# Kernel tuning notes

Hardware: AMD Instinct MI355X
Metric: run time of the kernel (lower is better)

Reference implementation:

```python
import jax, jax.numpy as jnp
import numpy as np

EMBED_DIM = 512
NUM_HEADS = 8
HEAD_DIM = EMBED_DIM // NUM_HEADS


def setup_inputs() -> dict:
    key = jax.random.key(0)
    k1, k2, kw, kb, kow, kob = jax.random.split(key, 6)
    B, L, C = 2, 2048, EMBED_DIM
    s = 1.0 / np.sqrt(C)
    return {
        "x1": jax.random.normal(k1, (B, L, C), dtype=jnp.float32),
        "x2": jax.random.normal(k2, (B, L, C), dtype=jnp.float32),
        # nn.Linear(embed_dim, 3*embed_dim): weight [3C, C], bias [3C]
        "qkv_w": jax.random.uniform(kw, (3 * C, C), jnp.float32, -s, s),
        "qkv_b": jax.random.uniform(kb, (3 * C,), jnp.float32, -s, s),
        # nn.Linear(embed_dim, embed_dim): weight [C, C], bias [C]
        "out_w": jax.random.uniform(kow, (C, C), jnp.float32, -s, s),
        "out_b": jax.random.uniform(kob, (C,), jnp.float32, -s, s),
    }


def _qkv(x, qkv_w, qkv_b):
    B, L, C = x.shape
    H, D = NUM_HEADS, C // NUM_HEADS
    # Linear: x @ W^T + b, then view(B, L, H, 3, D) and split along the '3' axis
    qkv = (jnp.einsum("blc,fc->blf", x, qkv_w) + qkv_b).reshape(B, L, H, 3, D)
    qkv = jnp.transpose(qkv, (3, 0, 2, 1, 4))  # [3, B, H, L, D]
    return qkv[0], qkv[1], qkv[2]


def _attend(q, k, v):
    # q,k,v: [B, H, L, D]; scale by 1/sqrt(D)
    scale = 1.0 / np.sqrt(q.shape[-1]).astype(np.float32)
    scores = jnp.einsum("bhqd,bhkd->bhqk", q, k) * scale  # [B,H,L,L]
    attn = jax.nn.softmax(scores, axis=-1)
    out = jnp.einsum("bhqk,bhkd->bhqd", attn, v)
    B, H, L, D = out.shape
    return jnp.transpose(out, (0, 2, 1, 3)).reshape(B, L, H * D)


def reference(x1, x2, qkv_w, qkv_b, out_w, out_b):
    q1, k1, v1 = _qkv(x1, qkv_w, qkv_b)
    q2, k2, v2 = _qkv(x2, qkv_w, qkv_b)
    out1 = _attend(q1, k2, v2)  # q from x1, k/v from x2
    out2 = _attend(q2, k1, v1)  # q from x2, k/v from x1
    out1 = jnp.einsum("blc,fc->blf", out1, out_w) + out_b
    out2 = jnp.einsum("blc,fc->blf", out2, out_w) + out_b
    return (out1, out2)
```

## Files before the change

kernel.cpp:

```cpp
#include <hip/hip_runtime.h>
#include <stdint.h>

typedef unsigned short u16;
typedef unsigned int u32;
typedef short bf16x8 __attribute__((ext_vector_type(8)));
typedef float f32x4 __attribute__((ext_vector_type(4)));
typedef float f32x16 __attribute__((ext_vector_type(16)));

#define K_DIM 512

__device__ __forceinline__ u16 f2bf(float f) {
  union { float f; u32 u; } v; v.f = f;
  return (u16)((v.u + 0x8000u) >> 16);
}
__device__ __forceinline__ u32 pk2(float lo, float hi) {
  union { float f; u32 u; } a, b; a.f = lo; b.f = hi;
  return __builtin_amdgcn_perm(b.u + 0x8000u, a.u + 0x8000u, 0x07060302u);
}

__global__ void cvt_kernel(const float* __restrict__ x1, const float* __restrict__ x2,
                           const float* __restrict__ qkvw, const float* __restrict__ outw,
                           u16* __restrict__ xb, u16* __restrict__ wqkv, u16* __restrict__ wout) {
  int tid = blockIdx.x * 256 + threadIdx.x;
  const float4* src; u16* dst; int idx = tid;
  if (idx < 524288)        { src = (const float4*)x1;   dst = xb; }
  else if (idx < 1048576)  { src = (const float4*)x2;   dst = xb + 2097152; idx -= 524288; }
  else if (idx < 1245184)  { src = (const float4*)qkvw; dst = wqkv;         idx -= 1048576; }
  else                     { src = (const float4*)outw; dst = wout;         idx -= 1245184; }
  float4 v = src[idx];
  *(uint2*)&dst[idx * 4] = make_uint2(pk2(v.x, v.y), pk2(v.z, v.w));
}

#define LDA 40

__global__ __launch_bounds__(256, 3) void qkv_gemm(
    const u16* __restrict__ A, const u16* __restrict__ W, const float* __restrict__ bias,
    u16* __restrict__ qb, u16* __restrict__ kb, u16* __restrict__ vtb) {
  __shared__ __align__(16) u16 As[2][128 * LDA];
  __shared__ __align__(16) u16 Bs[2][128 * LDA];
  const int t = threadIdx.x;
  const int m0 = blockIdx.x * 128, n0 = blockIdx.y * 128;
  const int lane = t & 63, l16 = lane & 15, quad = lane >> 4;
  const int w = t >> 6;
  const int wm = (w >> 1) * 64, wn = (w & 1) * 64;
  const int sr = t >> 2, sc = (t & 3) * 8;

  const u16* Ap = A + (size_t)(m0 + sr) * K_DIM + sc;
  const u16* Wp = W + (size_t)(n0 + sr) * K_DIM + sc;

  f32x4 acc[4][4];
#pragma unroll
  for (int i = 0; i < 4; ++i)
#pragma unroll
    for (int j = 0; j < 4; ++j) acc[i][j] = (f32x4){0.f, 0.f, 0.f, 0.f};

  uint4 ra0 = *(const uint4*)(Ap);
  uint4 ra1 = *(const uint4*)(Ap + 64 * K_DIM);
  uint4 rb0 = *(const uint4*)(Wp);
  uint4 rb1 = *(const uint4*)(Wp + 64 * K_DIM);
  *(uint4*)&As[0][sr * LDA + sc] = ra0;
  *(uint4*)&As[0][(sr + 64) * LDA + sc] = ra1;
  *(uint4*)&Bs[0][sr * LDA + sc] = rb0;
  *(uint4*)&Bs[0][(sr + 64) * LDA + sc] = rb1;
  ra0 = *(const uint4*)(Ap + 32);
  ra1 = *(const uint4*)(Ap + 64 * K_DIM + 32);
  rb0 = *(const uint4*)(Wp + 32);
  rb1 = *(const uint4*)(Wp + 64 * K_DIM + 32);
  __syncthreads();

  for (int kt = 0; kt < 16; ++kt) {
    const int cur = kt & 1, nxt = cur ^ 1;
    if (kt < 15) {
      *(uint4*)&As[nxt][sr * LDA + sc] = ra0;
      *(uint4*)&As[nxt][(sr + 64) * LDA + sc] = ra1;
      *(uint4*)&Bs[nxt][sr * LDA + sc] = rb0;
      *(uint4*)&Bs[nxt][(sr + 64) * LDA + sc] = rb1;
    }
    if (kt < 14) {
      int ko = (kt + 2) * 32;
      ra0 = *(const uint4*)(Ap + ko);
      ra1 = *(const uint4*)(Ap + 64 * K_DIM + ko);
      rb0 = *(const uint4*)(Wp + ko);
      rb1 = *(const uint4*)(Wp + 64 * K_DIM + ko);
    }
    bf16x8 af[4], bfr[4];
#pragma unroll
    for (int mi = 0; mi < 4; ++mi)
      af[mi] = *(const bf16x8*)&As[cur][(wm + mi * 16 + l16) * LDA + quad * 8];
#pragma unroll
    for (int ni = 0; ni < 4; ++ni)
      bfr[ni] = *(const bf16x8*)&Bs[cur][(wn + ni * 16 + l16) * LDA + quad * 8];
#pragma unroll
    for (int mi = 0; mi < 4; ++mi)
#pragma unroll
      for (int ni = 0; ni < 4; ++ni)
        acc[mi][ni] = __builtin_amdgcn_mfma_f32_16x16x32_bf16(bfr[ni], af[mi], acc[mi][ni], 0, 0, 0);
    __syncthreads();
  }

  const int fbase = n0 + wn;
  const int h = fbase / 192;
  const int s = (fbase - h * 192) >> 6;
  float4 bv[4];
#pragma unroll
  for (int ni = 0; ni < 4; ++ni)
    bv[ni] = *(const float4*)&bias[fbase + ni * 16 + quad * 4];
  const int bh = m0 >> 11;
  const int lbase = (m0 & 2047) + wm;

  if (s == 2) {
    u16* dst = vtb + (size_t)((bh * 8 + h) * 64) * 2048;
#pragma unroll
    for (int mi = 0; mi < 4; ++mi) {
      int l = lbase + mi * 16 + l16;
#pragma unroll
      for (int ni = 0; ni < 4; ++ni)
#pragma unroll
        for (int r = 0; r < 4; ++r)
          dst[(ni * 16 + quad * 4 + r) * 2048 + l] = f2bf(acc[mi][ni][r] + bv[ni][r]);
    }
  } else {
    u16* dst = (s == 0 ? qb : kb) + (size_t)((bh * 8 + h) * 2048) * 64;
    const float sc2 = (s == 0) ? 0.18033688011112042f : 1.0f;
#pragma unroll
    for (int mi = 0; mi < 4; ++mi) {
      int l = lbase + mi * 16 + l16;
#pragma unroll
      for (int ni = 0; ni < 4; ++ni) {
        float v0 = (acc[mi][ni][0] + bv[ni][0]) * sc2;
        float v1 = (acc[mi][ni][1] + bv[ni][1]) * sc2;
        float v2 = (acc[mi][ni][2] + bv[ni][2]) * sc2;
        float v3 = (acc[mi][ni][3] + bv[ni][3]) * sc2;
        *(uint2*)&dst[(size_t)l * 64 + ni * 16 + quad * 4] = make_uint2(pk2(v0, v1), pk2(v2, v3));
      }
    }
  }
}

#define LQ 72

#define SPHASE(SS, KBUF)                                                          \
  do {                                                                            \
    _Pragma("unroll") for (int r_ = 0; r_ < 16; ++r_) SS[r_] = 0.f;               \
    _Pragma("unroll") for (int ks_ = 0; ks_ < 4; ++ks_) {                         \
      bf16x8 kfr = *(const bf16x8*)&Ks[KBUF][(half32 + l32) * LQ + ks_ * 16 + h2 * 8]; \
      SS = __builtin_amdgcn_mfma_f32_32x32x16_bf16(kfr, qf[ks_], SS, 0, 0, 0);    \
    }                                                                             \
  } while (0)

#define SOFTPV(SS, VBUF)                                                          \
  do {                                                                            \
    float p[16];                                                                  \
    _Pragma("unroll") for (int r_ = 0; r_ < 16; ++r_)                             \
      p[r_] = __builtin_amdgcn_exp2f(SS[r_]);                                     \
    _Pragma("unroll") for (int r_ = 0; r_ < 16; r_ += 4)                          \
      rs += (p[r_] + p[r_ + 1]) + (p[r_ + 2] + p[r_ + 3]);                        \
    u32 a0 = pk2(p[0], p[1]),   b0 = pk2(p[2], p[3]);                             \
    u32 c0 = pk2(p[4], p[5]),   d0 = pk2(p[6], p[7]);                             \
    u32 a1 = pk2(p[8], p[9]),   b1 = pk2(p[10], p[11]);                           \
    u32 c1 = pk2(p[12], p[13]), d1 = pk2(p[14], p[15]);                           \
    asm("v_permlane32_swap_b32 %0, %1" : "+v"(a0), "+v"(c0));                     \
    asm("v_permlane32_swap_b32 %0, %1" : "+v"(b0), "+v"(d0));                     \
    asm("v_permlane32_swap_b32 %0, %1" : "+v"(a1), "+v"(c1));                     \
    asm("v_permlane32_swap_b32 %0, %1" : "+v"(b1), "+v"(d1));                     \
    union { u32 u[4]; bf16x8 v; } f0_, f1_;                                       \
    f0_.u[0] = a0; f0_.u[1] = b0; f0_.u[2] = c0; f0_.u[3] = d0;                   \
    f1_.u[0] = a1; f1_.u[1] = b1; f1_.u[2] = c1; f1_.u[3] = d1;                   \
    bf16x8 pf0 = f0_.v, pf1 = f1_.v;                                              \
    const u16* vb_ = (const u16*)VTs + (VBUF) * (64 * LQ);                        \
    bf16x8 vf0 = *(const bf16x8*)&vb_[l32 * LQ + half32 + h2 * 8];                \
    bf16x8 vf1 = *(const bf16x8*)&vb_[(32 + l32) * LQ + half32 + h2 * 8];         \
    oacc[0] = __builtin_amdgcn_mfma_f32_32x32x16_bf16(vf0, pf0, oacc[0], 0, 0, 0);\
    oacc[1] = __builtin_amdgcn_mfma_f32_32x32x16_bf16(vf1, pf0, oacc[1], 0, 0, 0);\
    vf0 = *(const bf16x8*)&vb_[l32 * LQ + half32 + 16 + h2 * 8];                  \
    vf1 = *(const bf16x8*)&vb_[(32 + l32) * LQ + half32 + 16 + h2 * 8];           \
    oacc[0] = __builtin_amdgcn_mfma_f32_32x32x16_bf16(vf0, pf1, oacc[0], 0, 0, 0);\
    oacc[1] = __builtin_amdgcn_mfma_f32_32x32x16_bf16(vf1, pf1, oacc[1], 0, 0, 0);\
  } while (0)

__global__ __launch_bounds__(512, 4) void attn_kernel(
    const u16* __restrict__ qb, const u16* __restrict__ kb, const u16* __restrict__ vtb,
    u16* __restrict__ attnb) {
  __shared__ __align__(16) u16 Ks[2][64 * LQ];
  __shared__ __align__(16) u16 VTs[4][64 * LQ];

  const int t = threadIdx.x;
  const int w = t >> 6, lane = t & 63, l32 = lane & 31, h2 = lane >> 5;
  const int qg = w & 3, half32 = (w >> 2) * 32;
  const int bid = blockIdx.x;
  const int comb = bid & 31;
  const int qt = bid >> 5;
  const int h = comb & 7, bb = (comb >> 3) & 1, pair = comb >> 4;
  const int in_q = pair, in_kv = pair ^ 1;

  const u16* Qg = qb + (size_t)((in_q * 2 + bb) * 8 + h) * 2048 * 64;
  const u16* Kg = kb + (size_t)((in_kv * 2 + bb) * 8 + h) * 2048 * 64;
  const u16* Vg = vtb + (size_t)((in_kv * 2 + bb) * 8 + h) * 64 * 2048;

  const int srow = t >> 3, sseg = (t & 7) * 8;
  uint4 rk0 = *(const uint4*)(Kg + srow * 64 + sseg);
  uint4 rv0 = *(const uint4*)(Vg + srow * 2048 + sseg);

  bf16x8 qf[4];
#pragma unroll
  for (int ks = 0; ks < 4; ++ks)
    qf[ks] = *(const bf16x8*)(Qg + (qt * 128 + qg * 32 + l32) * 64 + ks * 16 + h2 * 8);

  auto stage = [&](int kbuf, int vbuf) {
    *(uint4*)&Ks[kbuf][srow * LQ + sseg] = rk0;
    *(uint4*)&VTs[vbuf][srow * LQ + sseg] = rv0;
  };
  auto gload = [&](int kt) {
    const int ko = kt * 64;
    rk0 = *(const uint4*)(Kg + (ko + srow) * 64 + sseg);
    rv0 = *(const uint4*)(Vg + srow * 2048 + ko + sseg);
  };

  f32x16 oacc[2];
#pragma unroll
  for (int mi = 0; mi < 2; ++mi)
#pragma unroll
    for (int r = 0; r < 16; ++r) oacc[mi][r] = 0.f;
  float rs = 0.f;
  f32x16 sA, sB;

  stage(0, 0);
  gload(1);
  __syncthreads();

  SPHASE(sA, 0);
  stage(1, 1);
  gload(2);
  __syncthreads();

#pragma unroll 1
  for (int it = 0; it < 16; ++it) {
    const int e = (it & 1) << 1;
    SPHASE(sB, 1);
    SOFTPV(sA, e);
    if (it == 15) break;
    stage(0, e ^ 2);
    gload(2 * it + 3);
    __syncthreads();
    SPHASE(sA, 0);
    SOFTPV(sB, e + 1);
    stage(1, e ^ 3);
    if (it < 14) gload(2 * it + 4);
    __syncthreads();
  }
  SOFTPV(sB, 3);

  rs += __shfl_xor(rs, 32);
  __syncthreads();
  float* red = (float*)&VTs[0][0];
  float* rsb = red + 4 * 64 * 32;
  if (half32) {
#pragma unroll
    for (int mi = 0; mi < 2; ++mi)
#pragma unroll
      for (int r = 0; r < 16; ++r) {
        int d = mi * 32 + (r & 3) + 8 * (r >> 2) + 4 * h2;
        red[(qg * 64 + d) * 32 + l32] = oacc[mi][r];
      }
    if (lane < 32) rsb[qg * 32 + l32] = rs;
  }
  __syncthreads();
  if (!half32) {
#pragma unroll
    for (int mi = 0; mi < 2; ++mi)
#pragma unroll
      for (int r = 0; r < 16; ++r) {
        int d = mi * 32 + (r & 3) + 8 * (r >> 2) + 4 * h2;
        oacc[mi][r] += red[(qg * 64 + d) * 32 + l32];
      }
    rs += rsb[qg * 32 + l32];
    const float inv = 1.0f / rs;
    const int row = in_q * 4096 + bb * 2048 + qt * 128 + qg * 32 + l32;
#pragma unroll
    for (int mi = 0; mi < 2; ++mi)
#pragma unroll
      for (int rg = 0; rg < 4; ++rg) {
        float v0 = oacc[mi][rg * 4 + 0] * inv;
        float v1 = oacc[mi][rg * 4 + 1] * inv;
        float v2 = oacc[mi][rg * 4 + 2] * inv;
        float v3 = oacc[mi][rg * 4 + 3] * inv;
        *(uint2*)&attnb[(size_t)row * 512 + h * 64 + mi * 32 + rg * 8 + h2 * 4] =
            make_uint2(pk2(v0, v1), pk2(v2, v3));
      }
  }
}

__global__ __launch_bounds__(256, 2) void out_gemm(
    const u16* __restrict__ A, const u16* __restrict__ W, const float* __restrict__ bias,
    float* __restrict__ out) {
  __shared__ __align__(16) u16 As[2][64 * LDA];
  __shared__ __align__(16) u16 Bs[2][128 * LDA];
  const int t = threadIdx.x;
  const int m0 = blockIdx.x * 64, n0 = blockIdx.y * 128;
  const int lane = t & 63, l16 = lane & 15, quad = lane >> 4;
  const int w = t >> 6;
  const int wm = (w & 1) * 32, wn = (w >> 1) * 64;
  const int ar = t >> 2, ac = (t & 3) * 8;
  const int sr = t >> 2, sc = (t & 3) * 8;

  const u16* Ap = A + (size_t)(m0 + ar) * K_DIM + ac;
  const u16* Wp = W + (size_t)(n0 + sr) * K_DIM + sc;

  f32x4 acc[2][4];
#pragma unroll
  for (int i = 0; i < 2; ++i)
#pragma unroll
    for (int j = 0; j < 4; ++j) acc[i][j] = (f32x4){0.f, 0.f, 0.f, 0.f};

  uint4 ra = *(const uint4*)Ap;
  uint4 rb0 = *(const uint4*)(Wp);
  uint4 rb1 = *(const uint4*)(Wp + 64 * K_DIM);
  *(uint4*)&As[0][ar * LDA + ac] = ra;
  *(uint4*)&Bs[0][sr * LDA + sc] = rb0;
  *(uint4*)&Bs[0][(sr + 64) * LDA + sc] = rb1;
  ra = *(const uint4*)(Ap + 32);
  rb0 = *(const uint4*)(Wp + 32);
  rb1 = *(const uint4*)(Wp + 64 * K_DIM + 32);
  __syncthreads();

  for (int kt = 0; kt < 16; ++kt) {
    const int cur = kt & 1, nxt = cur ^ 1;
    if (kt < 15) {
      *(uint4*)&As[nxt][ar * LDA + ac] = ra;
      *(uint4*)&Bs[nxt][sr * LDA + sc] = rb0;
      *(uint4*)&Bs[nxt][(sr + 64) * LDA + sc] = rb1;
    }
    if (kt < 14) {
      int ko = (kt + 2) * 32;
      ra = *(const uint4*)(Ap + ko);
      rb0 = *(const uint4*)(Wp + ko);
      rb1 = *(const uint4*)(Wp + 64 * K_DIM + ko);
    }
    bf16x8 af[2], bfr[4];
#pragma unroll
    for (int mi = 0; mi < 2; ++mi)
      af[mi] = *(const bf16x8*)&As[cur][(wm + mi * 16 + l16) * LDA + quad * 8];
#pragma unroll
    for (int ni = 0; ni < 4; ++ni)
      bfr[ni] = *(const bf16x8*)&Bs[cur][(wn + ni * 16 + l16) * LDA + quad * 8];
#pragma unroll
    for (int mi = 0; mi < 2; ++mi)
#pragma unroll
      for (int ni = 0; ni < 4; ++ni)
        acc[mi][ni] = __builtin_amdgcn_mfma_f32_16x16x32_bf16(af[mi], bfr[ni], acc[mi][ni], 0, 0, 0);
    __syncthreads();
  }

#pragma unroll
  for (int ni = 0; ni < 4; ++ni) {
    int f = n0 + wn + ni * 16 + l16;
    float bv = bias[f];
#pragma unroll
    for (int mi = 0; mi < 2; ++mi)
#pragma unroll
      for (int r = 0; r < 4; ++r) {
        int m = m0 + wm + mi * 16 + quad * 4 + r;
        out[(size_t)m * 512 + f] = acc[mi][ni][r] + bv;
      }
  }
}

extern "C" void kernel_launch(void* const* d_in, const int* in_sizes, int n_in,
                              void* d_out, int out_size, void* d_ws, size_t ws_size,
                              hipStream_t stream) {
  const float* x1   = (const float*)d_in[0];
  const float* x2   = (const float*)d_in[1];
  const float* qkvw = (const float*)d_in[2];
  const float* qkvb = (const float*)d_in[3];
  const float* outw = (const float*)d_in[4];
  const float* outb = (const float*)d_in[5];
  float* out = (float*)d_out;
  char* ws = (char*)d_ws;

  u16* xb    = (u16*)(ws + 0);
  u16* wqkv  = (u16*)(ws + 8388608);
  u16* wout  = (u16*)(ws + 9961472);
  u16* qb    = (u16*)(ws + 10485760);
  u16* kb    = (u16*)(ws + 18874368);
  u16* vtb   = (u16*)(ws + 27262976);
  u16* attnb = (u16*)(ws + 0);

  cvt_kernel<<<5120, 256, 0, stream>>>(x1, x2, qkvw, outw, xb, wqkv, wout);

  dim3 g1(64, 12);
  qkv_gemm<<<g1, 256, 0, stream>>>(xb, wqkv, qkvb, qb, kb, vtb);

  attn_kernel<<<512, 512, 0, stream>>>(qb, kb, vtb, attnb);

  dim3 g3(128, 4);
  out_gemm<<<g3, 256, 0, stream>>>(attnb, wout, outb, out);
}
```

Measured before the change: 158.6 us.

## Load K fragments directly from global into registers, drop K shared staging

```diff
diff --git a/kernel.cpp b/kernel.cpp
--- a/kernel.cpp
+++ b/kernel.cpp
@@ -139,13 +139,20 @@
 
 #define LQ 72
 
-#define SPHASE(SS, KBUF)                                                          \
+#define LOADK(KF, KT)                                                             \
+  do {                                                                            \
+    const u16* kp_ = Kg + ((KT) * 64 + half32 + l32) * 64 + h2 * 8;               \
+    KF[0] = *(const bf16x8*)(kp_);                                                \
+    KF[1] = *(const bf16x8*)(kp_ + 16);                                           \
+    KF[2] = *(const bf16x8*)(kp_ + 32);                                           \
+    KF[3] = *(const bf16x8*)(kp_ + 48);                                           \
+  } while (0)
+
+#define SPHASE(SS, KF)                                                            \
   do {                                                                            \
     _Pragma("unroll") for (int r_ = 0; r_ < 16; ++r_) SS[r_] = 0.f;               \
-    _Pragma("unroll") for (int ks_ = 0; ks_ < 4; ++ks_) {                         \
-      bf16x8 kfr = *(const bf16x8*)&Ks[KBUF][(half32 + l32) * LQ + ks_ * 16 + h2 * 8]; \
-      SS = __builtin_amdgcn_mfma_f32_32x32x16_bf16(kfr, qf[ks_], SS, 0, 0, 0);    \
-    }                                                                             \
+    _Pragma("unroll") for (int ks_ = 0; ks_ < 4; ++ks_)                           \
+      SS = __builtin_amdgcn_mfma_f32_32x32x16_bf16(KF[ks_], qf[ks_], SS, 0, 0, 0);\
   } while (0)
 
 #define SOFTPV(SS, VBUF)                                                          \
@@ -181,7 +188,6 @@
 __global__ __launch_bounds__(512, 4) void attn_kernel(
     const u16* __restrict__ qb, const u16* __restrict__ kb, const u16* __restrict__ vtb,
     u16* __restrict__ attnb) {
-  __shared__ __align__(16) u16 Ks[2][64 * LQ];
   __shared__ __align__(16) u16 VTs[4][64 * LQ];
 
   const int t = threadIdx.x;
@@ -198,22 +204,22 @@
   const u16* Vg = vtb + (size_t)((in_kv * 2 + bb) * 8 + h) * 64 * 2048;
 
   const int srow = t >> 3, sseg = (t & 7) * 8;
-  uint4 rk0 = *(const uint4*)(Kg + srow * 64 + sseg);
   uint4 rv0 = *(const uint4*)(Vg + srow * 2048 + sseg);
+
+  bf16x8 kfA[4], kfB[4];
+  LOADK(kfA, 0);
+  LOADK(kfB, 1);
 
   bf16x8 qf[4];
 #pragma unroll
   for (int ks = 0; ks < 4; ++ks)
     qf[ks] = *(const bf16x8*)(Qg + (qt * 128 + qg * 32 + l32) * 64 + ks * 16 + h2 * 8);
 
-  auto stage = [&](int kbuf, int vbuf) {
-    *(uint4*)&Ks[kbuf][srow * LQ + sseg] = rk0;
+  auto stageV = [&](int vbuf) {
     *(uint4*)&VTs[vbuf][srow * LQ + sseg] = rv0;
   };
-  auto gload = [&](int kt) {
-    const int ko = kt * 64;
-    rk0 = *(const uint4*)(Kg + (ko + srow) * 64 + sseg);
-    rv0 = *(const uint4*)(Vg + srow * 2048 + ko + sseg);
+  auto gloadV = [&](int kt) {
+    rv0 = *(const uint4*)(Vg + srow * 2048 + kt * 64 + sseg);
   };
 
   f32x16 oacc[2];
@@ -224,28 +230,31 @@
   float rs = 0.f;
   f32x16 sA, sB;
 
-  stage(0, 0);
-  gload(1);
-  __syncthreads();
-
-  SPHASE(sA, 0);
-  stage(1, 1);
-  gload(2);
+  stageV(0);
+  gloadV(1);
+  __syncthreads();
+
+  SPHASE(sA, kfA);
+  LOADK(kfA, 2);
+  stageV(1);
+  gloadV(2);
   __syncthreads();
 
 #pragma unroll 1
   for (int it = 0; it < 16; ++it) {
     const int e = (it & 1) << 1;
-    SPHASE(sB, 1);
+    SPHASE(sB, kfB);
+    if (it < 15) LOADK(kfB, 2 * it + 3);
     SOFTPV(sA, e);
     if (it == 15) break;
-    stage(0, e ^ 2);
-    gload(2 * it + 3);
+    stageV(e ^ 2);
+    gloadV(2 * it + 3);
     __syncthreads();
-    SPHASE(sA, 0);
+    SPHASE(sA, kfA);
+    if (it < 14) LOADK(kfA, 2 * it + 4);
     SOFTPV(sB, e + 1);
-    stage(1, e ^ 3);
-    if (it < 14) gload(2 * it + 4);
+    stageV(e ^ 3);
+    if (it < 14) gloadV(2 * it + 4);
     __syncthreads();
   }
   SOFTPV(sB, 3);
```

Measured after the change: 290.1 us. +83.0%, slower.
